# Performance work log

Hardware: AMD Instinct MI355X
Metric: run time of the kernel (lower is better)

Reference implementation:

```python
import jax, jax.numpy as jnp
import numpy as np

# dims
B, T = 64, 512
L = 3                 # number of HMLSTM layers
IN = 512              # per-layer input size (all equal)
D = L * IN            # 1536 total input size
E = 1024              # embedding_size
H1, H2 = 1024, 1024   # linear_sizes
O = 512               # output_size


def setup_inputs() -> dict:
    key = jax.random.key(0)
    ks = jax.random.split(key, 12)
    s = 0.02
    return {
        "x": jax.random.normal(ks[0], (B, T, D), dtype=jnp.float32),
        # gate linears: Linear(sum(input_sizes) -> 1, bias=False), one per layer, stacked [L, D]
        "Wg": jax.random.normal(ks[1], (L, D), dtype=jnp.float32) * s,
        # per-layer embedding linears Linear(IN -> E), stacked [L, E, IN] / [L, E]
        "We": jax.random.normal(ks[2], (L, E, IN), dtype=jnp.float32) * s,
        "be": jax.random.normal(ks[3], (L, E), dtype=jnp.float32) * s,
        # tanh MLP stack
        "W1": jax.random.normal(ks[4], (H1, E), dtype=jnp.float32) * s,
        "b1": jax.random.normal(ks[5], (H1,), dtype=jnp.float32) * s,
        "W2": jax.random.normal(ks[6], (H2, H1), dtype=jnp.float32) * s,
        "b2": jax.random.normal(ks[7], (H2,), dtype=jnp.float32) * s,
        # output head
        "Wo": jax.random.normal(ks[8], (O, H2), dtype=jnp.float32) * s,
        "bo": jax.random.normal(ks[9], (O,), dtype=jnp.float32) * s,
    }


def reference(x, Wg, We, be, W1, b1, W2, b2, Wo, bo):
    b, t, d = x.shape
    h = x.reshape(b * t, d)                       # per-timestep features, fully batched over time
    # gates: sigmoid(Linear(full h -> 1)) per layer -> [N, L]
    g = jax.nn.sigmoid(h @ Wg.T)
    # split full input into per-layer chunks (equal sizes -> reshape) and gate them
    hl = h.reshape(b * t, L, IN) * g[:, :, None]  # [N, L, IN]
    # s = sum_l Linear_l(h_l * g_l); biases sum since each embedding adds its own bias
    s = jnp.einsum("nli,lei->ne", hl, We) + be.sum(axis=0)
    he = jax.nn.relu(s)
    # fnn: tanh-activated linear stack
    o = jnp.tanh(he @ W1.T + b1)
    o = jnp.tanh(o @ W2.T + b2)
    out = o @ Wo.T + bo
    return out.reshape(b, t, O)
```

## Files before the change

### kernel.cpp

```cpp
#include <hip/hip_runtime.h>
#include <math.h>


typedef __attribute__((ext_vector_type(8))) short short8;
typedef __attribute__((ext_vector_type(4))) float float4v;

#define DEV __device__ __forceinline__

DEV unsigned short f2bf(float f){
    union{float f; unsigned int i;} c; c.f = f;
    unsigned int r = c.i + 0x7fffu + ((c.i>>16)&1u);
    return (unsigned short)(r>>16);
}
DEV unsigned int pack2(float a, float b){
    return (unsigned int)f2bf(a) | ((unsigned int)f2bf(b)<<16);
}

DEV void gload_lds16(const unsigned short* g, unsigned short* l){
    __builtin_amdgcn_global_load_lds((const __attribute__((address_space(1))) void*)g,
                                     (__attribute__((address_space(3))) void*)l, 16, 0, 0);
}

__global__ __launch_bounds__(256) void prep(
    const float* __restrict__ x,  const float* __restrict__ Wg,
    const float* __restrict__ W1, const float* __restrict__ W2,
    const float* __restrict__ Wo, const float* __restrict__ We,
    unsigned short* __restrict__ u,   unsigned short* __restrict__ W1b,
    unsigned short* __restrict__ W2b, unsigned short* __restrict__ Wob,
    unsigned short* __restrict__ Wep)
{
    int b = blockIdx.x;
    if(b < 8192){
        int row  = b*4 + (threadIdx.x>>6);
        int lane = threadIdx.x & 63;
        const float4* xr = (const float4*)(x + (size_t)row*1536);
        float4 hv[6];
        #pragma unroll
        for(int j=0;j<6;j++) hv[j] = xr[j*64 + lane];

        float p[3];
        #pragma unroll
        for(int l=0;l<3;l++){
            const float4* wr = (const float4*)(Wg + (size_t)l*1536);
            float s = 0.f;
            #pragma unroll
            for(int j=0;j<6;j++){
                float4 wv = wr[j*64 + lane];
                s += hv[j].x*wv.x + hv[j].y*wv.y + hv[j].z*wv.z + hv[j].w*wv.w;
            }
            p[l] = s;
        }
        #pragma unroll
        for(int off=32; off; off>>=1){
            p[0] += __shfl_xor(p[0], off);
            p[1] += __shfl_xor(p[1], off);
            p[2] += __shfl_xor(p[2], off);
        }
        float g[3];
        #pragma unroll
        for(int l=0;l<3;l++) g[l] = 1.f/(1.f + __expf(-p[l]));

        uint2* ur = (uint2*)(u + (size_t)row*1536);
        #pragma unroll
        for(int j=0;j<6;j++){
            float gj = g[(j*64+lane)>>7];
            uint2 o;
            o.x = pack2(hv[j].x*gj, hv[j].y*gj);
            o.y = pack2(hv[j].z*gj, hv[j].w*gj);
            ur[j*64 + lane] = o;
        }
        return;
    }
    b -= 8192;
    if(b < 1280){
        const float* src; unsigned short* dst; int v0;
        if(b < 512)      { src = W1; dst = W1b; v0 = b<<8; }
        else if(b < 1024){ src = W2; dst = W2b; v0 = (b-512)<<8; }
        else             { src = Wo; dst = Wob; v0 = (b-1024)<<8; }
        int v = v0 + threadIdx.x;
        const float4* s = (const float4*)(src) + (size_t)v*2;
        float4 a = s[0], c = s[1];
        uint4 o;
        o.x = pack2(a.x, a.y); o.y = pack2(a.z, a.w);
        o.z = pack2(c.x, c.y); o.w = pack2(c.z, c.w);
        *((uint4*)dst + v) = o;
        return;
    }
    b -= 1280;
    int v  = b*256 + threadIdx.x;
    int i8 = v & 63;
    int e  = (v>>6) & 1023;
    int l  = v>>16;
    const float4* s = (const float4*)(We + (size_t)l*524288 + (size_t)e*512 + i8*8);
    float4 a = s[0], c = s[1];
    uint4 o;
    o.x = pack2(a.x, a.y); o.y = pack2(a.z, a.w);
    o.z = pack2(c.x, c.y); o.w = pack2(c.z, c.w);
    *(uint4*)(Wep + (size_t)e*1536 + (size_t)l*512 + i8*8) = o;
}

template<int ACT, int BIAS_ROWS, bool F32OUT>
__global__ __launch_bounds__(512, 2) void gemm256(
    const unsigned short* __restrict__ A,
    const unsigned short* __restrict__ W,
    const float* __restrict__ bias,
    void* __restrict__ Cv,
    int M, int N, int K)
{
    __shared__ __align__(128) unsigned short As[2*2*128*64];
    __shared__ __align__(128) unsigned short Bs[2*2*128*64];

    const int tid = threadIdx.x;
    const int nb  = N >> 8;
    const int mt  = M >> 8;
    const int xcd = blockIdx.x & 7;
    const int j   = blockIdx.x >> 3;
    const int bm  = xcd*(mt>>3) + j/nb;
    const int bn  = j % nb;
    const int m0  = bm << 8, n0 = bn << 8;

    const int lane = tid & 63, wid = tid >> 6;
    const int wm = wid >> 2, wn = wid & 3;
    const int lr = lane & 15, quad = lane >> 4, sx = lr & 7;
    const int srow = lane >> 3;
    const int scb  = (lane & 7) ^ srow;
    const size_t aoff = (size_t)srow*K + scb*8;
    const int nt = K >> 6;

    float4v acc[8][4];
    #pragma unroll
    for(int i=0;i<8;i++)
        #pragma unroll
        for(int jj=0;jj<4;jj++) acc[i][jj] = (float4v){0.f,0.f,0.f,0.f};

#define STAGE_A(h,l,s,P) gload_lds16(A + ((size_t)(m0 + (h)*128 + (l)*64 + wid*8))*K + (size_t)(s)*64 + aoff, \
                                     &As[((P)*2+(h))*8192 + ((l)*64 + wid*8)*64])
#define STAGE_B(h,l,s,P) gload_lds16(W + ((size_t)(n0 + (h)*128 + (l)*64 + wid*8))*K + (size_t)(s)*64 + aoff, \
                                     &Bs[((P)*2+(h))*8192 + ((l)*64 + wid*8)*64])

    STAGE_A(0,0,0,0); STAGE_A(0,1,0,0); STAGE_A(1,0,0,0); STAGE_A(1,1,0,0);
    STAGE_B(0,0,0,0); STAGE_B(0,1,0,0); STAGE_B(1,0,0,0); STAGE_B(1,1,0,0);
    STAGE_B(0,0,1,1); STAGE_B(0,1,1,1); STAGE_B(1,0,1,1); STAGE_B(1,1,1,1);
    STAGE_A(0,0,1,1); STAGE_A(1,0,1,1);
    asm volatile("s_waitcnt vmcnt(6)" ::: "memory");
    __builtin_amdgcn_s_barrier();

    for(int tt=0; tt<nt; tt+=2){
        #pragma unroll
        for(int uu=0; uu<2; ++uu){
            const int T = tt + uu;
            const unsigned short* Ab = &As[(uu*2 + wm)*8192];
            const unsigned short* Bb = &Bs[(uu*2 + (wn>>1))*8192 + (wn&1)*4096];
            short8 bfr[4][2];
            #pragma unroll
            for(int q=0; q<4; ++q){
                short8 af[2][2];
                #pragma unroll
                for(int mi=0; mi<2; ++mi)
                    #pragma unroll
                    for(int ks=0; ks<2; ++ks)
                        af[mi][ks] = *(const short8*)&Ab[(q*32 + mi*16 + lr)*64 + (((ks*4+quad)^sx)*8)];
                if(q==0){
                    #pragma unroll
                    for(int ni=0; ni<4; ++ni)
                        #pragma unroll
                        for(int ks=0; ks<2; ++ks)
                            bfr[ni][ks] = *(const short8*)&Bb[(ni*16 + lr)*64 + (((ks*4+quad)^sx)*8)];
                }
                if(q==0)      { if(T+1 < nt){ STAGE_A(0,1,T+1,1-uu); STAGE_A(1,1,T+1,1-uu); } }
                else if(q==1) { if(T+2 < nt){ STAGE_B(0,0,T+2,uu);   STAGE_B(0,1,T+2,uu);   } }
                else if(q==2) { if(T+2 < nt){ STAGE_B(1,0,T+2,uu);   STAGE_B(1,1,T+2,uu);   } }
                else          { if(T+2 < nt){ STAGE_A(0,0,T+2,uu);   STAGE_A(1,0,T+2,uu);   } }
                if(q==0) asm volatile("s_waitcnt lgkmcnt(8)");
                __builtin_amdgcn_s_barrier();
                asm volatile("s_waitcnt lgkmcnt(0)");
                __builtin_amdgcn_s_setprio(1);
                #pragma unroll
                for(int ks=0; ks<2; ++ks)
                    #pragma unroll
                    for(int mi=0; mi<2; ++mi)
                        #pragma unroll
                        for(int ni=0; ni<4; ++ni)
                            acc[q*2+mi][ni] = __builtin_amdgcn_mfma_f32_16x16x32_bf16(
                                af[mi][ks], bfr[ni][ks], acc[q*2+mi][ni], 0, 0, 0);
                __builtin_amdgcn_s_setprio(0);
                if(q < 3) __builtin_amdgcn_s_barrier();
            }
            if(T+2 < nt) asm volatile("s_waitcnt vmcnt(6)" ::: "memory");
            else         asm volatile("s_waitcnt vmcnt(0)" ::: "memory");
            __builtin_amdgcn_s_barrier();
        }
    }
#undef STAGE_A
#undef STAGE_B

    #pragma unroll
    for(int ni=0; ni<4; ++ni){
        const int n = n0 + wn*64 + ni*16 + lr;
        float bsum = 0.f;
        #pragma unroll
        for(int r=0; r<BIAS_ROWS; ++r) bsum += bias[(size_t)r*N + n];
        #pragma unroll
        for(int Q=0; Q<8; ++Q){
            #pragma unroll
            for(int reg=0; reg<4; ++reg){
                const int m = m0 + wm*128 + Q*16 + quad*4 + reg;
                float v = acc[Q][ni][reg] + bsum;
                if(ACT==1)      v = fmaxf(v, 0.f);
                else if(ACT==2) v = tanhf(v);
                if constexpr (F32OUT) ((float*)Cv)[(size_t)m*N + n] = v;
                else                  ((unsigned short*)Cv)[(size_t)m*N + n] = f2bf(v);
            }
        }
    }
}

extern "C" void kernel_launch(void* const* d_in, const int* in_sizes, int n_in,
                              void* d_out, int out_size, void* d_ws, size_t ws_size,
                              hipStream_t stream)
{
    const float* x  = (const float*)d_in[0];
    const float* Wg = (const float*)d_in[1];
    const float* We = (const float*)d_in[2];
    const float* be = (const float*)d_in[3];
    const float* W1 = (const float*)d_in[4];
    const float* b1 = (const float*)d_in[5];
    const float* W2 = (const float*)d_in[6];
    const float* b2 = (const float*)d_in[7];
    const float* Wo = (const float*)d_in[8];
    const float* bo = (const float*)d_in[9];
    float* out = (float*)d_out;

    const int M = 32768;

    char* w = (char*)d_ws;
    unsigned short* Wep   = (unsigned short*)w; w += (size_t)1024*1536*2;
    unsigned short* W1b   = (unsigned short*)w; w += (size_t)1024*1024*2;
    unsigned short* W2b   = (unsigned short*)w; w += (size_t)1024*1024*2;
    unsigned short* Wob   = (unsigned short*)w; w += (size_t)512*1024*2;
    unsigned short* slotA = (unsigned short*)w; w += (size_t)M*1536*2;
    unsigned short* slotB = (unsigned short*)w; w += (size_t)M*1024*2;
    unsigned short* u  = slotA;
    unsigned short* o1 = slotA;
    unsigned short* he = slotB;
    unsigned short* o2 = slotB;

    hipLaunchKernelGGL(prep, dim3(10240), dim3(256), 0, stream,
                       x, Wg, W1, W2, Wo, We, u, W1b, W2b, Wob, Wep);

    hipLaunchKernelGGL((gemm256<1,3,false>), dim3((M/256)*(1024/256)), dim3(512), 0, stream,
                       u,  Wep, be, he,  M, 1024, 1536);
    hipLaunchKernelGGL((gemm256<2,1,false>), dim3((M/256)*(1024/256)), dim3(512), 0, stream,
                       he, W1b, b1, o1,  M, 1024, 1024);
    hipLaunchKernelGGL((gemm256<2,1,false>), dim3((M/256)*(1024/256)), dim3(512), 0, stream,
                       o1, W2b, b2, o2,  M, 1024, 1024);
    hipLaunchKernelGGL((gemm256<0,1,true>),  dim3((M/256)*(512/256)),  dim3(512), 0, stream,
                       o2, Wob, bo, out, M, 512, 1024);
}
```

Measured before the change: 652.4 us.

## Simplify GEMM mainloop to one barrier per k-tile with register-prefetched A fragments

Replaces the fine-grained per-quarter staging schedule, which issued global-to-LDS loads across four sub-phases with barriers between them, with a simpler double buffer. All loads for tile T+1 are issued at the start of iteration T, and only one barrier per k-tile is kept. A fragments are read from LDS into registers ahead of the MFMA groups that need them, so LDS reads interleave with MFMAs. This cuts the number of barriers, but it raises register pressure and waits for all outstanding global loads (vmcnt(0)) at each tile end, so the loads get less lead time to hide latency.

```diff
diff --git a/kernel.cpp b/kernel.cpp
--- a/kernel.cpp
+++ b/kernel.cpp
@@ -137,62 +137,71 @@
                                      &As[((P)*2+(h))*8192 + ((l)*64 + wid*8)*64])
 #define STAGE_B(h,l,s,P) gload_lds16(W + ((size_t)(n0 + (h)*128 + (l)*64 + wid*8))*K + (size_t)(s)*64 + aoff, \
                                      &Bs[((P)*2+(h))*8192 + ((l)*64 + wid*8)*64])
-
-    STAGE_A(0,0,0,0); STAGE_A(0,1,0,0); STAGE_A(1,0,0,0); STAGE_A(1,1,0,0);
-    STAGE_B(0,0,0,0); STAGE_B(0,1,0,0); STAGE_B(1,0,0,0); STAGE_B(1,1,0,0);
-    STAGE_B(0,0,1,1); STAGE_B(0,1,1,1); STAGE_B(1,0,1,1); STAGE_B(1,1,1,1);
-    STAGE_A(0,0,1,1); STAGE_A(1,0,1,1);
-    asm volatile("s_waitcnt vmcnt(6)" ::: "memory");
+#define STAGE_ALL(s,P) do{ \
+    STAGE_A(0,0,s,P); STAGE_A(0,1,s,P); STAGE_A(1,0,s,P); STAGE_A(1,1,s,P); \
+    STAGE_B(0,0,s,P); STAGE_B(0,1,s,P); STAGE_B(1,0,s,P); STAGE_B(1,1,s,P); }while(0)
+
+    STAGE_ALL(0,0);
+    asm volatile("s_waitcnt vmcnt(0)" ::: "memory");
     __builtin_amdgcn_s_barrier();
 
     for(int tt=0; tt<nt; tt+=2){
         #pragma unroll
         for(int uu=0; uu<2; ++uu){
             const int T = tt + uu;
+            if(T+1 < nt) STAGE_ALL(T+1, 1-uu);
+
             const unsigned short* Ab = &As[(uu*2 + wm)*8192];
             const unsigned short* Bb = &Bs[(uu*2 + (wn>>1))*8192 + (wn&1)*4096];
-            short8 bfr[4][2];
-            #pragma unroll
-            for(int q=0; q<4; ++q){
-                short8 af[2][2];
+
+            short8 bfr[4][2], af[4][2][2];
+            #pragma unroll
+            for(int ni=0; ni<4; ++ni)
+                #pragma unroll
+                for(int ks=0; ks<2; ++ks)
+                    bfr[ni][ks] = *(const short8*)&Bb[(ni*16 + lr)*64 + (((ks*4+quad)^sx)*8)];
+            #pragma unroll
+            for(int q=0; q<2; ++q)
                 #pragma unroll
                 for(int mi=0; mi<2; ++mi)
                     #pragma unroll
                     for(int ks=0; ks<2; ++ks)
-                        af[mi][ks] = *(const short8*)&Ab[(q*32 + mi*16 + lr)*64 + (((ks*4+quad)^sx)*8)];
-                if(q==0){
-                    #pragma unroll
-                    for(int ni=0; ni<4; ++ni)
-                        #pragma unroll
-                        for(int ks=0; ks<2; ++ks)
-                            bfr[ni][ks] = *(const short8*)&Bb[(ni*16 + lr)*64 + (((ks*4+quad)^sx)*8)];
-                }
-                if(q==0)      { if(T+1 < nt){ STAGE_A(0,1,T+1,1-uu); STAGE_A(1,1,T+1,1-uu); } }
-                else if(q==1) { if(T+2 < nt){ STAGE_B(0,0,T+2,uu);   STAGE_B(0,1,T+2,uu);   } }
-                else if(q==2) { if(T+2 < nt){ STAGE_B(1,0,T+2,uu);   STAGE_B(1,1,T+2,uu);   } }
-                else          { if(T+2 < nt){ STAGE_A(0,0,T+2,uu);   STAGE_A(1,0,T+2,uu);   } }
-                if(q==0) asm volatile("s_waitcnt lgkmcnt(8)");
-                __builtin_amdgcn_s_barrier();
-                asm volatile("s_waitcnt lgkmcnt(0)");
-                __builtin_amdgcn_s_setprio(1);
-                #pragma unroll
-                for(int ks=0; ks<2; ++ks)
-                    #pragma unroll
-                    for(int mi=0; mi<2; ++mi)
-                        #pragma unroll
-                        for(int ni=0; ni<4; ++ni)
-                            acc[q*2+mi][ni] = __builtin_amdgcn_mfma_f32_16x16x32_bf16(
-                                af[mi][ks], bfr[ni][ks], acc[q*2+mi][ni], 0, 0, 0);
-                __builtin_amdgcn_s_setprio(0);
-                if(q < 3) __builtin_amdgcn_s_barrier();
-            }
-            if(T+2 < nt) asm volatile("s_waitcnt vmcnt(6)" ::: "memory");
-            else         asm volatile("s_waitcnt vmcnt(0)" ::: "memory");
+                        af[q][mi][ks] = *(const short8*)&Ab[(q*32 + mi*16 + lr)*64 + (((ks*4+quad)^sx)*8)];
+
+#define MFMAQ(q) do{ \
+    __builtin_amdgcn_s_setprio(1); \
+    _Pragma("unroll") \
+    for(int ks=0; ks<2; ++ks) \
+        _Pragma("unroll") \
+        for(int mi=0; mi<2; ++mi) \
+            _Pragma("unroll") \
+            for(int ni=0; ni<4; ++ni) \
+                acc[(q)*2+mi][ni] = __builtin_amdgcn_mfma_f32_16x16x32_bf16( \
+                    af[q][mi][ks], bfr[ni][ks], acc[(q)*2+mi][ni], 0, 0, 0); \
+    __builtin_amdgcn_s_setprio(0); }while(0)
+#define READA(q) do{ \
+    _Pragma("unroll") \
+    for(int mi=0; mi<2; ++mi) \
+        _Pragma("unroll") \
+        for(int ks=0; ks<2; ++ks) \
+            af[q][mi][ks] = *(const short8*)&Ab[((q)*32 + mi*16 + lr)*64 + (((ks*4+quad)^sx)*8)]; }while(0)
+
+            MFMAQ(0);
+            READA(2);
+            MFMAQ(1);
+            READA(3);
+            MFMAQ(2);
+            MFMAQ(3);
+#undef MFMAQ
+#undef READA
+
+            if(T+1 < nt) asm volatile("s_waitcnt vmcnt(0)" ::: "memory");
             __builtin_amdgcn_s_barrier();
         }
     }
 #undef STAGE_A
 #undef STAGE_B
+#undef STAGE_ALL
 
     #pragma unroll
     for(int ni=0; ni<4; ++ni){
```

Result: slower. 667.7 us (+2.3%).

## Replace 256x256 GEMM with 128x256 tile, 4-wave, K=32 double-buffered kernel

Applied to the files above, without the earlier changes.

Rewrites the GEMM kernel to use 256-thread blocks with a 128x256 output tile and a K-step of 32 instead of 64, using a simpler double-buffered pipeline that prefetches the full next stage at once and syncs once per step. Each wave now owns a 128x64 column strip, reads B fragments once and streams A fragments interleaved with MFMAs. This cuts the LDS footprint and barrier count per tile and may allow more resident blocks. In exchange it lowers data reuse per block, doubles the number of K iterations, and waits with vmcnt(0) on every step, which exposes more load latency.

```diff
diff --git a/kernel.cpp b/kernel.cpp
--- a/kernel.cpp
+++ b/kernel.cpp
@@ -100,32 +100,32 @@
 }
 
 template<int ACT, int BIAS_ROWS, bool F32OUT>
-__global__ __launch_bounds__(512, 2) void gemm256(
+__global__ __launch_bounds__(256, 2) void gemm_bt2(
     const unsigned short* __restrict__ A,
     const unsigned short* __restrict__ W,
     const float* __restrict__ bias,
     void* __restrict__ Cv,
     int M, int N, int K)
 {
-    __shared__ __align__(128) unsigned short As[2*2*128*64];
-    __shared__ __align__(128) unsigned short Bs[2*2*128*64];
+    __shared__ __align__(128) unsigned short As[2*128*32];
+    __shared__ __align__(128) unsigned short Bs[2*256*32];
 
     const int tid = threadIdx.x;
     const int nb  = N >> 8;
-    const int mt  = M >> 8;
+    const int mt  = M >> 7;
     const int xcd = blockIdx.x & 7;
     const int j   = blockIdx.x >> 3;
     const int bm  = xcd*(mt>>3) + j/nb;
     const int bn  = j % nb;
-    const int m0  = bm << 8, n0 = bn << 8;
+    const int m0  = bm << 7, n0 = bn << 8;
 
     const int lane = tid & 63, wid = tid >> 6;
-    const int wm = wid >> 2, wn = wid & 3;
-    const int lr = lane & 15, quad = lane >> 4, sx = lr & 7;
-    const int srow = lane >> 3;
-    const int scb  = (lane & 7) ^ srow;
-    const size_t aoff = (size_t)srow*K + scb*8;
-    const int nt = K >> 6;
+    const int lr = lane & 15, quad = lane >> 4;
+    const int cread = ((quad ^ (lr & 3)) * 8);
+    const int rl  = lane >> 2;
+    const int cbl = (lane & 3) ^ (rl & 3);
+    const size_t aoff = (size_t)rl*K + cbl*8;
+    const int nt = K >> 5;
 
     float4v acc[8][4];
     #pragma unroll
@@ -133,70 +133,62 @@
         #pragma unroll
         for(int jj=0;jj<4;jj++) acc[i][jj] = (float4v){0.f,0.f,0.f,0.f};
 
-#define STAGE_A(h,l,s,P) gload_lds16(A + ((size_t)(m0 + (h)*128 + (l)*64 + wid*8))*K + (size_t)(s)*64 + aoff, \
-                                     &As[((P)*2+(h))*8192 + ((l)*64 + wid*8)*64])
-#define STAGE_B(h,l,s,P) gload_lds16(W + ((size_t)(n0 + (h)*128 + (l)*64 + wid*8))*K + (size_t)(s)*64 + aoff, \
-                                     &Bs[((P)*2+(h))*8192 + ((l)*64 + wid*8)*64])
-
-    STAGE_A(0,0,0,0); STAGE_A(0,1,0,0); STAGE_A(1,0,0,0); STAGE_A(1,1,0,0);
-    STAGE_B(0,0,0,0); STAGE_B(0,1,0,0); STAGE_B(1,0,0,0); STAGE_B(1,1,0,0);
-    STAGE_B(0,0,1,1); STAGE_B(0,1,1,1); STAGE_B(1,0,1,1); STAGE_B(1,1,1,1);
-    STAGE_A(0,0,1,1); STAGE_A(1,0,1,1);
-    asm volatile("s_waitcnt vmcnt(6)" ::: "memory");
+#define STAGE_A(d,s,P) gload_lds16(A + ((size_t)(m0 + (wid*2+(d))*16))*K + (size_t)(s)*32 + aoff, \
+                                   &As[(P)*4096 + ((wid*2+(d))*16)*32])
+#define STAGE_B(d,s,P) gload_lds16(W + ((size_t)(n0 + (wid*4+(d))*16))*K + (size_t)(s)*32 + aoff, \
+                                   &Bs[(P)*8192 + ((wid*4+(d))*16)*32])
+#define STAGE_ALL(s,P) do{ STAGE_A(0,s,P); STAGE_A(1,s,P); \
+    STAGE_B(0,s,P); STAGE_B(1,s,P); STAGE_B(2,s,P); STAGE_B(3,s,P); }while(0)
+
+#define READ_AF(mi) af[mi] = *(const short8*)&Ap[(mi)*512 + lr*32 + cread]
+#define MFMA_MI(mi) do{ \
+    acc[mi][0] = __builtin_amdgcn_mfma_f32_16x16x32_bf16(af[mi], bfr[0], acc[mi][0], 0,0,0); \
+    acc[mi][1] = __builtin_amdgcn_mfma_f32_16x16x32_bf16(af[mi], bfr[1], acc[mi][1], 0,0,0); \
+    acc[mi][2] = __builtin_amdgcn_mfma_f32_16x16x32_bf16(af[mi], bfr[2], acc[mi][2], 0,0,0); \
+    acc[mi][3] = __builtin_amdgcn_mfma_f32_16x16x32_bf16(af[mi], bfr[3], acc[mi][3], 0,0,0); }while(0)
+
+    STAGE_ALL(0,0);
+    asm volatile("s_waitcnt vmcnt(0)" ::: "memory");
     __builtin_amdgcn_s_barrier();
 
     for(int tt=0; tt<nt; tt+=2){
         #pragma unroll
         for(int uu=0; uu<2; ++uu){
             const int T = tt + uu;
-            const unsigned short* Ab = &As[(uu*2 + wm)*8192];
-            const unsigned short* Bb = &Bs[(uu*2 + (wn>>1))*8192 + (wn&1)*4096];
-            short8 bfr[4][2];
-            #pragma unroll
-            for(int q=0; q<4; ++q){
-                short8 af[2][2];
-                #pragma unroll
-                for(int mi=0; mi<2; ++mi)
-                    #pragma unroll
-                    for(int ks=0; ks<2; ++ks)
-                        af[mi][ks] = *(const short8*)&Ab[(q*32 + mi*16 + lr)*64 + (((ks*4+quad)^sx)*8)];
-                if(q==0){
-                    #pragma unroll
-                    for(int ni=0; ni<4; ++ni)
-                        #pragma unroll
-                        for(int ks=0; ks<2; ++ks)
-                            bfr[ni][ks] = *(const short8*)&Bb[(ni*16 + lr)*64 + (((ks*4+quad)^sx)*8)];
-                }
-                if(q==0)      { if(T+1 < nt){ STAGE_A(0,1,T+1,1-uu); STAGE_A(1,1,T+1,1-uu); } }
-                else if(q==1) { if(T+2 < nt){ STAGE_B(0,0,T+2,uu);   STAGE_B(0,1,T+2,uu);   } }
-                else if(q==2) { if(T+2 < nt){ STAGE_B(1,0,T+2,uu);   STAGE_B(1,1,T+2,uu);   } }
-                else          { if(T+2 < nt){ STAGE_A(0,0,T+2,uu);   STAGE_A(1,0,T+2,uu);   } }
-                if(q==0) asm volatile("s_waitcnt lgkmcnt(8)");
+            if(T+1 < nt) STAGE_ALL(T+1, 1-uu);
+            __builtin_amdgcn_sched_barrier(0);
+
+            const unsigned short* Ap = &As[uu*4096];
+            const unsigned short* Bp = &Bs[uu*8192 + wid*2048];
+            short8 af[8], bfr[4];
+            bfr[0] = *(const short8*)&Bp[        lr*32 + cread];
+            bfr[1] = *(const short8*)&Bp[ 512 +  lr*32 + cread];
+            bfr[2] = *(const short8*)&Bp[1024 +  lr*32 + cread];
+            bfr[3] = *(const short8*)&Bp[1536 +  lr*32 + cread];
+            READ_AF(0); READ_AF(1); READ_AF(2); READ_AF(3);
+            __builtin_amdgcn_s_setprio(1);
+            MFMA_MI(0); READ_AF(4);
+            MFMA_MI(1); READ_AF(5);
+            MFMA_MI(2); READ_AF(6);
+            MFMA_MI(3); READ_AF(7);
+            MFMA_MI(4); MFMA_MI(5); MFMA_MI(6); MFMA_MI(7);
+            __builtin_amdgcn_s_setprio(0);
+
+            if(T+1 < nt){
+                asm volatile("s_waitcnt vmcnt(0)" ::: "memory");
                 __builtin_amdgcn_s_barrier();
-                asm volatile("s_waitcnt lgkmcnt(0)");
-                __builtin_amdgcn_s_setprio(1);
-                #pragma unroll
-                for(int ks=0; ks<2; ++ks)
-                    #pragma unroll
-                    for(int mi=0; mi<2; ++mi)
-                        #pragma unroll
-                        for(int ni=0; ni<4; ++ni)
-                            acc[q*2+mi][ni] = __builtin_amdgcn_mfma_f32_16x16x32_bf16(
-                                af[mi][ks], bfr[ni][ks], acc[q*2+mi][ni], 0, 0, 0);
-                __builtin_amdgcn_s_setprio(0);
-                if(q < 3) __builtin_amdgcn_s_barrier();
             }
-            if(T+2 < nt) asm volatile("s_waitcnt vmcnt(6)" ::: "memory");
-            else         asm volatile("s_waitcnt vmcnt(0)" ::: "memory");
-            __builtin_amdgcn_s_barrier();
         }
     }
 #undef STAGE_A
 #undef STAGE_B
+#undef STAGE_ALL
+#undef READ_AF
+#undef MFMA_MI
 
     #pragma unroll
     for(int ni=0; ni<4; ++ni){
-        const int n = n0 + wn*64 + ni*16 + lr;
+        const int n = n0 + wid*64 + ni*16 + lr;
         float bsum = 0.f;
         #pragma unroll
         for(int r=0; r<BIAS_ROWS; ++r) bsum += bias[(size_t)r*N + n];
@@ -204,7 +196,7 @@
         for(int Q=0; Q<8; ++Q){
             #pragma unroll
             for(int reg=0; reg<4; ++reg){
-                const int m = m0 + wm*128 + Q*16 + quad*4 + reg;
+                const int m = m0 + Q*16 + quad*4 + reg;
                 float v = acc[Q][ni][reg] + bsum;
                 if(ACT==1)      v = fmaxf(v, 0.f);
                 else if(ACT==2) v = tanhf(v);
@@ -248,12 +240,12 @@
     hipLaunchKernelGGL(prep, dim3(10240), dim3(256), 0, stream,
                        x, Wg, W1, W2, Wo, We, u, W1b, W2b, Wob, Wep);
 
-    hipLaunchKernelGGL((gemm256<1,3,false>), dim3((M/256)*(1024/256)), dim3(512), 0, stream,
+    hipLaunchKernelGGL((gemm_bt2<1,3,false>), dim3((M/128)*(1024/256)), dim3(256), 0, stream,
                        u,  Wep, be, he,  M, 1024, 1536);
-    hipLaunchKernelGGL((gemm256<2,1,false>), dim3((M/256)*(1024/256)), dim3(512), 0, stream,
+    hipLaunchKernelGGL((gemm_bt2<2,1,false>), dim3((M/128)*(1024/256)), dim3(256), 0, stream,
                        he, W1b, b1, o1,  M, 1024, 1024);
-    hipLaunchKernelGGL((gemm256<2,1,false>), dim3((M/256)*(1024/256)), dim3(512), 0, stream,
+    hipLaunchKernelGGL((gemm_bt2<2,1,false>), dim3((M/128)*(1024/256)), dim3(256), 0, stream,
                        o1, W2b, b2, o2,  M, 1024, 1024);
-    hipLaunchKernelGGL((gemm256<0,1,true>),  dim3((M/256)*(512/256)),  dim3(512), 0, stream,
+    hipLaunchKernelGGL((gemm_bt2<0,1,true>),  dim3((M/128)*(512/256)),  dim3(256), 0, stream,
                        o2, Wob, bo, out, M, 512, 1024);
 }
```

Result: slower. 678.8 us (+4.0%).
